# Optimization experiments

Measured on AMD Instinct MI355X. Metric: run time of the kernel, lower is better.

## Reference

```python
import jax, jax.numpy as jnp
import numpy as np

N, C, K, P = 262144, 64, 27, 131072
EPS = 1e-5


def setup_inputs() -> dict:
    key = jax.random.key(0)
    ks = jax.random.split(key, 8)
    x = jax.random.normal(ks[0], (N, C), jnp.float32)
    W1 = jax.random.normal(ks[1], (K, C, C), jnp.float32) * 0.05
    b1 = jax.random.normal(ks[2], (C,), jnp.float32) * 0.05
    W2 = jax.random.normal(ks[3], (K, C, C), jnp.float32) * 0.05
    b2 = jax.random.normal(ks[4], (C,), jnp.float32) * 0.05
    gamma1 = jnp.ones((C,), jnp.float32)
    beta1 = jnp.zeros((C,), jnp.float32)
    gamma2 = jnp.ones((C,), jnp.float32)
    beta2 = jnp.zeros((C,), jnp.float32)
    in_idx = jax.random.randint(ks[5], (K, P), 0, N, jnp.int32)
    out_idx = jax.random.randint(ks[6], (K, P), 0, N, jnp.int32)
    return dict(x=x, W1=W1, b1=b1, gamma1=gamma1, beta1=beta1,
                W2=W2, b2=b2, gamma2=gamma2, beta2=beta2,
                in_idx=in_idx, out_idx=out_idx)


def sparse_conv(x, W, b, in_idx, out_idx):
    """Rulebook sparse conv: for each kernel offset k, gather rows, GEMM, scatter-add."""
    out0 = jnp.zeros((x.shape[0], W.shape[-1]), x.dtype)

    def step(out, kslice):
        Wk, ik, ok = kslice
        msg = x[ik] @ Wk                      # [P, C] gather + GEMM
        return out.at[ok].add(msg), None      # scatter-add

    out, _ = jax.lax.scan(step, out0, (W, in_idx, out_idx))
    return out + b


def batchnorm(h, gamma, beta):
    # training-mode BatchNorm1d over node rows (biased variance)
    mean = h.mean(axis=0)
    var = h.var(axis=0)
    return (h - mean) * jax.lax.rsqrt(var + EPS) * gamma + beta


def reference(x, W1, b1, gamma1, beta1, W2, b2, gamma2, beta2, in_idx, out_idx):
    h = jax.nn.relu(batchnorm(sparse_conv(x, W1, b1, in_idx, out_idx), gamma1, beta1))
    h = batchnorm(sparse_conv(h, W2, b2, in_idx, out_idx), gamma2, beta2)
    return jax.nn.relu(h + x)  # identity shortcut (in_planes == planes, stride == 1)
```

## Files before the change

### kernel.cpp

```cpp
#include <hip/hip_runtime.h>
#include <hip/hip_bf16.h>


#define NNODES 262144
#define NC 64
#define NK 27
#define NP 131072
#define NPAIR (NK * NP)
#define EPSV 1e-5f
#define TILE 64
#define TPB 4
#define BGRID 2048

typedef float f32x4 __attribute__((ext_vector_type(4)));
typedef __bf16 bf16x8 __attribute__((ext_vector_type(8)));

__global__ void prep_w(const float* __restrict__ W, __bf16* __restrict__ Wt) {
    int i = blockIdx.x * 256 + threadIdx.x;
    if (i >= NK * NC * NC) return;
    int k  = i >> 12;
    int n  = (i >> 6) & 63;
    int ci = i & 63;
    Wt[i] = (__bf16)W[k * 4096 + ci * 64 + n];
}

__global__ __launch_bounds__(256) void prep_x(const float* __restrict__ X, __bf16* __restrict__ Xb) {
    size_t i = (size_t)(blockIdx.x * 256 + threadIdx.x) * 8;
    f32x4 a = *(const f32x4*)(X + i);
    f32x4 b = *(const f32x4*)(X + i + 4);
    bf16x8 o;
#pragma unroll
    for (int j = 0; j < 4; ++j) { o[j] = (__bf16)a[j]; o[4 + j] = (__bf16)b[j]; }
    *(bf16x8*)(Xb + i) = o;
}

__global__ void rank_kernel(const int* __restrict__ ok, int* __restrict__ hist, int* __restrict__ rank) {
    int i = blockIdx.x * 256 + threadIdx.x;
    rank[i] = atomicAdd(&hist[ok[i]], 1);
}

__global__ __launch_bounds__(256) void scan1(const int* __restrict__ hist, int* __restrict__ start,
                                             int* __restrict__ bsum) {
    __shared__ int sh[256];
    const int b = blockIdx.x, t = threadIdx.x;
    int4 v = *(const int4*)(hist + b * 1024 + t * 4);
    int s0 = v.x, s1 = s0 + v.y, s2 = s1 + v.z, s3 = s2 + v.w;
    sh[t] = s3;
    __syncthreads();
    for (int off = 1; off < 256; off <<= 1) {
        int val = (t >= off) ? sh[t - off] : 0;
        __syncthreads();
        sh[t] += val;
        __syncthreads();
    }
    int excl = (t == 0) ? 0 : sh[t - 1];
    if (t == 255) bsum[b] = sh[255];
    int4 o;
    o.x = excl; o.y = excl + s0; o.z = excl + s1; o.w = excl + s2;
    *(int4*)(start + b * 1024 + t * 4) = o;
}

__global__ __launch_bounds__(256) void scan2(int* __restrict__ bsum) {
    __shared__ int sh[256];
    const int t = threadIdx.x;
    sh[t] = bsum[t];
    __syncthreads();
    for (int off = 1; off < 256; off <<= 1) {
        int val = (t >= off) ? sh[t - off] : 0;
        __syncthreads();
        sh[t] += val;
        __syncthreads();
    }
    bsum[t] = (t == 0) ? 0 : sh[t - 1];
}

__global__ __launch_bounds__(256) void scan3(int* __restrict__ start, const int* __restrict__ bsum) {
    const int b = blockIdx.x, t = threadIdx.x;
    int add = bsum[b];
    int4 v = *(int4*)(start + b * 1024 + t * 4);
    v.x += add; v.y += add; v.z += add; v.w += add;
    *(int4*)(start + b * 1024 + t * 4) = v;
    if (b == 0 && t == 0) start[NNODES] = NPAIR;
}

__global__ void perm_kernel(const int* __restrict__ ok, const int* __restrict__ start,
                            int* __restrict__ rank) {
    int i = blockIdx.x * 256 + threadIdx.x;
    rank[i] = start[ok[i]] + rank[i];
}

__global__ __launch_bounds__(256) void bin_count(const int* __restrict__ ok, int* __restrict__ bhist,
                                                 int shiftC, int ncc) {
    __shared__ int lcount[32];
    int p = blockIdx.x * 256 + threadIdx.x;
    int k = p >> 17;
    int c = ok[p] >> shiftC;
    if (threadIdx.x < ncc) lcount[threadIdx.x] = 0;
    __syncthreads();
    atomicAdd(&lcount[c], 1);
    __syncthreads();
    if (threadIdx.x < ncc) {
        int n = lcount[threadIdx.x];
        if (n > 0) atomicAdd(&bhist[k * ncc + threadIdx.x], n);
    }
}

__global__ __launch_bounds__(1024) void bin_scan(const int* __restrict__ bhist,
                                                 int* __restrict__ bstart, int NB) {
    __shared__ int sh[1024];
    const int t = threadIdx.x;
    int own = (t < NB) ? bhist[t] : 0;
    sh[t] = own;
    __syncthreads();
    for (int off = 1; off < 1024; off <<= 1) {
        int val = (t >= off) ? sh[t - off] : 0;
        __syncthreads();
        sh[t] += val;
        __syncthreads();
    }
    if (t < NB) bstart[t] = sh[t] - own;
    if (t == 0) bstart[NB] = NPAIR;
}

__global__ __launch_bounds__(256) void bin_fill(const int* __restrict__ ik, const int* __restrict__ ok,
                                                const int* __restrict__ perm, const int* __restrict__ start,
                                                const int* __restrict__ bstart, int* __restrict__ bhist2,
                                                int* __restrict__ cin, int* __restrict__ cslot,
                                                int shiftC, int ncc) {
    __shared__ int lcount[32];
    __shared__ int lbase[32];
    int p = blockIdx.x * 256 + threadIdx.x;
    int k = p >> 17;
    int c = ok[p] >> shiftC;
    if (threadIdx.x < ncc) lcount[threadIdx.x] = 0;
    __syncthreads();
    int pos = atomicAdd(&lcount[c], 1);
    __syncthreads();
    if (threadIdx.x < ncc) {
        int n = lcount[threadIdx.x];
        lbase[threadIdx.x] = (n > 0) ? atomicAdd(&bhist2[k * ncc + threadIdx.x], n) : 0;
    }
    __syncthreads();
    int rec = bstart[k * ncc + c] + lbase[c] + pos;
    cin[rec]   = ik[p];
    cslot[rec] = perm[p] - start[c << shiftC];
}

template <bool BN>
__global__ __launch_bounds__(256)
void phaseA(const __bf16* __restrict__ Xb, const __bf16* __restrict__ Wt,
            const int* __restrict__ cin, const int* __restrict__ cslot,
            const int* __restrict__ bstart, const float* __restrict__ st,
            __bf16* __restrict__ msg, int ncc, int chunk, int capr) {
    const int k   = blockIdx.y;
    const int bin = k * ncc + chunk;
    const int b0  = bstart[bin];
    const int b1  = bstart[bin + 1];
    const int base = b0 + blockIdx.x * (TILE * TPB);
    if (base >= b1) return;

    const int tid  = threadIdx.x;
    const int wave = tid >> 6;
    const int lane = tid & 63;
    const int l15  = lane & 15;
    const int l4   = lane >> 4;

    __shared__ __align__(16) __bf16 As[64 * 64];
    __shared__ __align__(16) __bf16 Cs[64 * 64];
    __shared__ float s_s[64], s_t[64];

    if (BN && tid < 64) { s_s[tid] = st[tid]; s_t[tid] = st[64 + tid]; }

    bf16x8 bfrag[4][2];
    const __bf16* Wk = Wt + k * 4096;
#pragma unroll
    for (int nt = 0; nt < 4; ++nt)
#pragma unroll
        for (int ks = 0; ks < 2; ++ks)
            bfrag[nt][ks] = *(const bf16x8*)(Wk + (nt * 16 + l15) * 64 + ks * 32 + l4 * 8);

    const int r = tid >> 2;
    const int q = tid & 3;
    char* Ab = (char*)As;
    char* Cb = (char*)Cs;
    const int rb = wave * 16;

    __syncthreads();

    for (int t = 0; t < TPB; ++t) {
        const int p0 = base + t * TILE;
        if (p0 >= b1) break;
        const int rec   = p0 + r;
        const bool valid = rec < b1;
        const int gidx = valid ? cin[rec] : 0;
        const int slot = valid ? cslot[rec] : capr + r;

        const __bf16* xr = Xb + (size_t)gidx * 64 + q * 16;
        bf16x8 c0 = *(const bf16x8*)xr;
        bf16x8 c1 = *(const bf16x8*)(xr + 8);
        if (BN) {
            const int cb = q * 16;
#pragma unroll
            for (int j = 0; j < 8; ++j) {
                float v0 = (float)c0[j], v1 = (float)c1[j];
                c0[j] = (__bf16)fmaxf(fmaf(v0, s_s[cb + j],     s_t[cb + j]),     0.0f);
                c1[j] = (__bf16)fmaxf(fmaf(v1, s_s[cb + 8 + j], s_t[cb + 8 + j]), 0.0f);
            }
        }
        *(bf16x8*)(Ab + r * 128 + (((2 * q)     ^ (r & 7)) << 4)) = c0;
        *(bf16x8*)(Ab + r * 128 + (((2 * q + 1) ^ (r & 7)) << 4)) = c1;
        __syncthreads();

        f32x4 acc[4];
#pragma unroll
        for (int nt = 0; nt < 4; ++nt)
#pragma unroll
            for (int j = 0; j < 4; ++j) acc[nt][j] = 0.0f;
#pragma unroll
        for (int ks = 0; ks < 2; ++ks) {
            const int row = rb + l15;
            bf16x8 a = *(const bf16x8*)(Ab + row * 128 + ((((ks << 2) + l4) ^ (row & 7)) << 4));
#pragma unroll
            for (int nt = 0; nt < 4; ++nt)
                acc[nt] = __builtin_amdgcn_mfma_f32_16x16x32_bf16(a, bfrag[nt][ks], acc[nt], 0, 0, 0);
        }

#pragma unroll
        for (int rg = 0; rg < 4; ++rg) {
            const int row = rb + l4 * 4 + rg;
            char* cr = Cb + row * 128;
#pragma unroll
            for (int nt = 0; nt < 4; ++nt) {
                const int ch = nt * 2 + (l15 >> 3);
                *(__bf16*)(cr + ((ch ^ (row & 7)) << 4) + (l15 & 7) * 2) = (__bf16)acc[nt][rg];
            }
        }
        __syncthreads();

        bf16x8 o0 = *(bf16x8*)(Cb + r * 128 + (((2 * q)     ^ (r & 7)) << 4));
        bf16x8 o1 = *(bf16x8*)(Cb + r * 128 + (((2 * q + 1) ^ (r & 7)) << 4));
        __bf16* mr = msg + (size_t)slot * 64 + q * 16;
        *(bf16x8*)mr       = o0;
        *(bf16x8*)(mr + 8) = o1;
    }
}

template <bool FIRST>
__global__ __launch_bounds__(256)
void phaseB(const __bf16* __restrict__ msg, const int* __restrict__ start,
            int cbase, int nodesC,
            __bf16* __restrict__ outb, float* __restrict__ outf, float* __restrict__ psum) {
    const int wave = threadIdx.x >> 6;
    const int lane = threadIdx.x & 63;
    const int rs   = lane >> 3;
    const int g    = lane & 7;
    const int slotbase = start[cbase];
    float s[8], s2[8];
#pragma unroll
    for (int j = 0; j < 8; ++j) { s[j] = 0.0f; s2[j] = 0.0f; }

    for (int n0 = blockIdx.x * 4 + wave; n0 < nodesC; n0 += gridDim.x * 4) {
        const int n = cbase + n0;
        const int b = start[n] - slotbase;
        const int deg = start[n + 1] - slotbase - b;
        float acc[8];
#pragma unroll
        for (int j = 0; j < 8; ++j) acc[j] = 0.0f;
        for (int i = rs; i < deg; i += 8) {
            bf16x8 v = *(const bf16x8*)(msg + (size_t)(b + i) * 64 + g * 8);
#pragma unroll
            for (int j = 0; j < 8; ++j) acc[j] += (float)v[j];
        }
#pragma unroll
        for (int j = 0; j < 8; ++j) {
            acc[j] += __shfl_xor(acc[j], 8);
            acc[j] += __shfl_xor(acc[j], 16);
            acc[j] += __shfl_xor(acc[j], 32);
        }
        if (rs == 0) {
            if (FIRST) {
                bf16x8 o;
#pragma unroll
                for (int j = 0; j < 8; ++j) o[j] = (__bf16)acc[j];
                *(bf16x8*)(outb + (size_t)n * 64 + g * 8) = o;
            } else {
                f32x4 o0, o1;
#pragma unroll
                for (int j = 0; j < 4; ++j) { o0[j] = acc[j]; o1[j] = acc[4 + j]; }
                *(f32x4*)(outf + (size_t)n * 64 + g * 8)     = o0;
                *(f32x4*)(outf + (size_t)n * 64 + g * 8 + 4) = o1;
            }
#pragma unroll
            for (int j = 0; j < 8; ++j) { s[j] += acc[j]; s2[j] += acc[j] * acc[j]; }
        }
    }

    __shared__ float reds[4][64], reds2[4][64];
    if (rs == 0) {
#pragma unroll
        for (int j = 0; j < 8; ++j) { reds[wave][g * 8 + j] = s[j]; reds2[wave][g * 8 + j] = s2[j]; }
    }
    __syncthreads();
    if (threadIdx.x < 64) {
        const int c = threadIdx.x;
        float ts  = reds[0][c] + reds[1][c] + reds[2][c] + reds[3][c];
        float ts2 = reds2[0][c] + reds2[1][c] + reds2[2][c] + reds2[3][c];
        float* pr = psum + (size_t)blockIdx.x * 128;
        pr[c]      += ts;
        pr[64 + c] += ts2;
    }
}

__global__ __launch_bounds__(256) void bn_reduce(const float* __restrict__ psum, float* __restrict__ sums) {
    const int m = blockIdx.x;
    float s = 0.0f;
    for (int b = threadIdx.x; b < BGRID; b += 256) s += psum[(size_t)b * 128 + m];
    __shared__ float sh[256];
    sh[threadIdx.x] = s;
    __syncthreads();
    for (int off = 128; off > 0; off >>= 1) {
        if (threadIdx.x < off) sh[threadIdx.x] += sh[threadIdx.x + off];
        __syncthreads();
    }
    if (threadIdx.x == 0) sums[m] = sh[0];
}

__global__ void bn_params(const float* __restrict__ sums, const float* __restrict__ gamma,
                          const float* __restrict__ beta, float* __restrict__ st) {
    int c = threadIdx.x;
    const float inv = 1.0f / (float)NNODES;
    float mean = sums[c] * inv;
    float var  = sums[64 + c] * inv - mean * mean;
    float s    = gamma[c] * rsqrtf(var + EPSV);
    st[c]      = s;
    st[64 + c] = beta[c] - mean * s;
}

__global__ __launch_bounds__(256)
void final_kernel(float* __restrict__ Out, const float* __restrict__ X, const float* __restrict__ st) {
    __shared__ float s_s[64], s_t[64];
    if (threadIdx.x < 64) { s_s[threadIdx.x] = st[threadIdx.x]; s_t[threadIdx.x] = st[64 + threadIdx.x]; }
    __syncthreads();
    int i = blockIdx.x * 256 + threadIdx.x;
    f32x4 h  = *(f32x4*)(Out + (size_t)i * 4);
    f32x4 xv = *(const f32x4*)(X + (size_t)i * 4);
    const int cb = (i & 15) * 4;
    f32x4 o;
#pragma unroll
    for (int j = 0; j < 4; ++j)
        o[j] = fmaxf(fmaf(h[j], s_s[cb + j], s_t[cb + j]) + xv[j], 0.0f);
    *(f32x4*)(Out + (size_t)i * 4) = o;
}

template <bool BN>
__global__ __launch_bounds__(256)
void conv_kernel(const float* __restrict__ X, const __bf16* __restrict__ Wt,
                 const int* __restrict__ in_idx, const int* __restrict__ out_idx,
                 const float* __restrict__ st, float* __restrict__ Out) {
    const int k    = blockIdx.y;
    const int tid  = threadIdx.x;
    const int wave = tid >> 6;
    const int lane = tid & 63;
    const int l15  = lane & 15;
    const int l4   = lane >> 4;
    __shared__ __align__(16) __bf16 As[64 * 64];
    __shared__ int oks[TILE];
    __shared__ float s_s[64], s_t[64];
    if (BN && tid < 64) { s_s[tid] = st[tid]; s_t[tid] = st[64 + tid]; }
    bf16x8 bfrag[4][2];
    const __bf16* Wk = Wt + k * 4096;
#pragma unroll
    for (int nt = 0; nt < 4; ++nt)
#pragma unroll
        for (int ks = 0; ks < 2; ++ks)
            bfrag[nt][ks] = *(const bf16x8*)(Wk + (nt * 16 + l15) * 64 + ks * 32 + l4 * 8);
    const int* ik = in_idx + k * NP;
    const int* ok = out_idx + k * NP;
    const int r = tid >> 2;
    const int q = tid & 3;
    char* Abase = (char*)As;
    const int rb = wave * 16;
    __syncthreads();
    int p0 = (blockIdx.x * 8) * TILE;
    for (int t = 0; t < 8; ++t, p0 += TILE) {
        if (tid < TILE) oks[tid] = ok[p0 + tid];
        const float* xr = X + (size_t)ik[p0 + r] * 64 + q * 16;
        f32x4 v0 = *(const f32x4*)(xr + 0);
        f32x4 v1 = *(const f32x4*)(xr + 4);
        f32x4 v2 = *(const f32x4*)(xr + 8);
        f32x4 v3 = *(const f32x4*)(xr + 12);
        float vals[16];
        *(f32x4*)&vals[0]  = v0; *(f32x4*)&vals[4]  = v1;
        *(f32x4*)&vals[8]  = v2; *(f32x4*)&vals[12] = v3;
        if (BN) {
            const int cb = q * 16;
#pragma unroll
            for (int j = 0; j < 16; ++j)
                vals[j] = fmaxf(fmaf(vals[j], s_s[cb + j], s_t[cb + j]), 0.0f);
        }
        bf16x8 c0, c1;
#pragma unroll
        for (int j = 0; j < 8; ++j) { c0[j] = (__bf16)vals[j]; c1[j] = (__bf16)vals[8 + j]; }
        *(bf16x8*)(Abase + r * 128 + (((2 * q)     ^ (r & 7)) << 4)) = c0;
        *(bf16x8*)(Abase + r * 128 + (((2 * q + 1) ^ (r & 7)) << 4)) = c1;
        __syncthreads();
        f32x4 acc[4];
#pragma unroll
        for (int nt = 0; nt < 4; ++nt)
#pragma unroll
            for (int j = 0; j < 4; ++j) acc[nt][j] = 0.0f;
#pragma unroll
        for (int ks = 0; ks < 2; ++ks) {
            const int row = rb + l15;
            bf16x8 a = *(const bf16x8*)(Abase + row * 128 + ((((ks << 2) + l4) ^ (row & 7)) << 4));
#pragma unroll
            for (int nt = 0; nt < 4; ++nt)
                acc[nt] = __builtin_amdgcn_mfma_f32_16x16x32_bf16(a, bfrag[nt][ks], acc[nt], 0, 0, 0);
        }
#pragma unroll
        for (int rg = 0; rg < 4; ++rg) {
            const int rr = rb + l4 * 4 + rg;
            float* orow = Out + (size_t)oks[rr] * 64;
#pragma unroll
            for (int nt = 0; nt < 4; ++nt)
                unsafeAtomicAdd(orow + nt * 16 + l15, acc[nt][rg]);
        }
        __syncthreads();
    }
}

__global__ __launch_bounds__(256)
void bn_stats(const float* __restrict__ H, float* __restrict__ sums) {
    const int c    = threadIdx.x & 63;
    const int slot = threadIdx.x >> 6;
    float s = 0.0f, s2 = 0.0f;
    for (int row = blockIdx.x * 4 + slot; row < NNODES; row += gridDim.x * 4) {
        float v = H[(size_t)row * 64 + c];
        s += v; s2 += v * v;
    }
    __shared__ float red[8][64];
    red[slot][c] = s; red[4 + slot][c] = s2;
    __syncthreads();
    if (slot == 0) {
        s  = red[0][c] + red[1][c] + red[2][c] + red[3][c];
        s2 = red[4][c] + red[5][c] + red[6][c] + red[7][c];
        unsafeAtomicAdd(&sums[c], s);
        unsafeAtomicAdd(&sums[64 + c], s2);
    }
}

extern "C" void kernel_launch(void* const* d_in, const int* in_sizes, int n_in,
                              void* d_out, int out_size, void* d_ws, size_t ws_size,
                              hipStream_t stream) {
    const float* x      = (const float*)d_in[0];
    const float* W1     = (const float*)d_in[1];
    const float* gamma1 = (const float*)d_in[3];
    const float* beta1  = (const float*)d_in[4];
    const float* W2     = (const float*)d_in[5];
    const float* gamma2 = (const float*)d_in[7];
    const float* beta2  = (const float*)d_in[8];
    const int* in_idx   = (const int*)d_in[9];
    const int* out_idx  = (const int*)d_in[10];
    float* out = (float*)d_out;

    char* ws = (char*)d_ws;

    auto plan_bytes = [&](int ncc) -> size_t {
        auto rup = [](size_t b) { return (b + 255) & ~(size_t)255; };
        size_t capr = (size_t)NPAIR / ncc + 65536;
        size_t tot = 0;
        tot += rup((capr + 64) * 128);
        tot += rup((size_t)NNODES * 64 * 2);
        tot += rup((size_t)NNODES * 64 * 2);
        tot += rup((size_t)NPAIR * 4);
        tot += rup((size_t)NPAIR * 4);
        tot += rup((size_t)NPAIR * 4);
        tot += rup((size_t)NNODES * 4);
        tot += rup((size_t)(NNODES + 64) * 4);
        tot += rup((size_t)NK * ncc * 4) * 2;
        tot += rup((size_t)(NK * ncc + 1) * 4);
        tot += rup(1024);
        tot += rup((size_t)NK * 4096 * 2) * 2;
        tot += rup((size_t)BGRID * 128 * 4) * 2;
        tot += rup(512) * 4;
        return tot;
    };
    int ncc = -1;
    const int cands[4] = {4, 8, 16, 32};
    for (int ci = 0; ci < 4; ++ci)
        if (plan_bytes(cands[ci]) <= ws_size) { ncc = cands[ci]; break; }

    if (ncc > 0) {
        const int shiftC = 18 - __builtin_ctz(ncc);
        const int NB     = NK * ncc;
        const int capr   = NPAIR / ncc + 65536;
        const int nodesC = NNODES / ncc;

        size_t off = 0;
        auto alloc = [&](size_t bytes) -> char* {
            char* p = ws + off;
            off = (off + bytes + 255) & ~(size_t)255;
            return p;
        };
        __bf16* msg    = (__bf16*)alloc((size_t)(capr + 64) * 128);
        __bf16* xbf    = (__bf16*)alloc((size_t)NNODES * 64 * 2);
        __bf16* h1bf   = (__bf16*)alloc((size_t)NNODES * 64 * 2);
        int*    perm   = (int*)alloc((size_t)NPAIR * 4);
        int*    cin    = (int*)alloc((size_t)NPAIR * 4);
        int*    cslot  = (int*)alloc((size_t)NPAIR * 4);
        int*    hist   = (int*)alloc((size_t)NNODES * 4);
        int*    startv = (int*)alloc((size_t)(NNODES + 64) * 4);
        int*    bhist  = (int*)alloc((size_t)NB * 4);
        int*    bhist2 = (int*)alloc((size_t)NB * 4);
        int*    bstart = (int*)alloc((size_t)(NB + 1) * 4);
        int*    bsum   = (int*)alloc(1024);
        __bf16* Wt1    = (__bf16*)alloc((size_t)NK * 4096 * 2);
        __bf16* Wt2    = (__bf16*)alloc((size_t)NK * 4096 * 2);
        float*  psumA  = (float*)alloc((size_t)BGRID * 128 * 4);
        float*  psumB  = (float*)alloc((size_t)BGRID * 128 * 4);
        float*  sums1  = (float*)alloc(512);
        float*  st1    = (float*)alloc(512);
        float*  sums2  = (float*)alloc(512);
        float*  st2    = (float*)alloc(512);

        (void)hipMemsetAsync(hist, 0, (size_t)NNODES * 4, stream);
        (void)hipMemsetAsync(bhist, 0, (size_t)NB * 4, stream);
        (void)hipMemsetAsync(bhist2, 0, (size_t)NB * 4, stream);
        (void)hipMemsetAsync(psumA, 0, (size_t)BGRID * 128 * 4, stream);
        (void)hipMemsetAsync(psumB, 0, (size_t)BGRID * 128 * 4, stream);

        prep_x<<<NNODES * 64 / 8 / 256, 256, 0, stream>>>(x, xbf);
        prep_w<<<(NK * NC * NC + 255) / 256, 256, 0, stream>>>(W1, Wt1);
        prep_w<<<(NK * NC * NC + 255) / 256, 256, 0, stream>>>(W2, Wt2);

        rank_kernel<<<NPAIR / 256, 256, 0, stream>>>(out_idx, hist, perm);
        scan1<<<256, 256, 0, stream>>>(hist, startv, bsum);
        scan2<<<1, 256, 0, stream>>>(bsum);
        scan3<<<256, 256, 0, stream>>>(startv, bsum);
        perm_kernel<<<NPAIR / 256, 256, 0, stream>>>(out_idx, startv, perm);
        bin_count<<<NPAIR / 256, 256, 0, stream>>>(out_idx, bhist, shiftC, ncc);
        bin_scan<<<1, 1024, 0, stream>>>(bhist, bstart, NB);
        bin_fill<<<NPAIR / 256, 256, 0, stream>>>(in_idx, out_idx, perm, startv, bstart,
                                                  bhist2, cin, cslot, shiftC, ncc);

        const int meanbin = NP / ncc;
        const int cover   = meanbin + ((meanbin / 8 > 512) ? meanbin / 8 : 512);
        const int bx      = (cover + TILE * TPB - 1) / (TILE * TPB);
        dim3 agrid(bx, NK);

        for (int c = 0; c < ncc; ++c) {
            phaseA<false><<<agrid, 256, 0, stream>>>(xbf, Wt1, cin, cslot, bstart,
                                                     nullptr, msg, ncc, c, capr);
            phaseB<true><<<BGRID, 256, 0, stream>>>(msg, startv, c * nodesC, nodesC,
                                                    h1bf, nullptr, psumA);
        }
        bn_reduce<<<128, 256, 0, stream>>>(psumA, sums1);
        bn_params<<<1, 64, 0, stream>>>(sums1, gamma1, beta1, st1);
        for (int c = 0; c < ncc; ++c) {
            phaseA<true><<<agrid, 256, 0, stream>>>(h1bf, Wt2, cin, cslot, bstart,
                                                    st1, msg, ncc, c, capr);
            phaseB<false><<<BGRID, 256, 0, stream>>>(msg, startv, c * nodesC, nodesC,
                                                     nullptr, out, psumB);
        }
        bn_reduce<<<128, 256, 0, stream>>>(psumB, sums2);
        bn_params<<<1, 64, 0, stream>>>(sums2, gamma2, beta2, st2);
        final_kernel<<<NNODES * 64 / 4 / 256, 256, 0, stream>>>(out, x, st2);
    } else {
        size_t o2 = 0;
        auto alloc2 = [&](size_t bytes) -> char* {
            char* p = ws + o2;
            o2 = (o2 + bytes + 255) & ~(size_t)255;
            return p;
        };
        float*  h1    = (float*)alloc2((size_t)NNODES * 64 * 4);
        float*  fsums1= (float*)alloc2(512);
        float*  fst1  = (float*)alloc2(512);
        float*  fsums2= (float*)alloc2(512);
        float*  fst2  = (float*)alloc2(512);
        __bf16* fWt1  = (__bf16*)alloc2((size_t)NK * 4096 * 2);
        __bf16* fWt2  = (__bf16*)alloc2((size_t)NK * 4096 * 2);

        (void)hipMemsetAsync(h1, 0, (size_t)NNODES * 64 * 4, stream);
        (void)hipMemsetAsync(fsums1, 0, 512, stream);
        (void)hipMemsetAsync(fsums2, 0, 512, stream);
        (void)hipMemsetAsync(d_out, 0, (size_t)out_size * 4, stream);

        prep_w<<<(NK * NC * NC + 255) / 256, 256, 0, stream>>>(W1, fWt1);
        prep_w<<<(NK * NC * NC + 255) / 256, 256, 0, stream>>>(W2, fWt2);
        dim3 cgrid(NP / TILE / 8, NK);
        conv_kernel<false><<<cgrid, 256, 0, stream>>>(x, fWt1, in_idx, out_idx, nullptr, h1);
        bn_stats<<<1024, 256, 0, stream>>>(h1, fsums1);
        bn_params<<<1, 64, 0, stream>>>(fsums1, gamma1, beta1, fst1);
        conv_kernel<true><<<cgrid, 256, 0, stream>>>(h1, fWt2, in_idx, out_idx, fst1, out);
        bn_stats<<<1024, 256, 0, stream>>>(out, fsums2);
        bn_params<<<1, 64, 0, stream>>>(fsums2, gamma2, beta2, fst2);
        final_kernel<<<NNODES * 64 / 4 / 256, 256, 0, stream>>>(out, x, fst2);
    }
}
```

Before: 998.4 us.

## Fuse preprocessing kernels into one launch and enlarge phaseA tiles per block

Merges x/W bf16 conversion, the rank histogram and the bin count into a single multi-role kernel, and folds the perm computation into bin_fill, which removes several launches and one pass over out_idx. It also doubles tiles per block in phaseA, shrinks the message-buffer slack, and raises the minimum bin coverage. The smaller capr slack could overflow if a bin exceeds the mean by more than 16384 pairs, and larger blocks reduce the number of blocks in the grid.

```diff
diff --git a/kernel.cpp b/kernel.cpp
--- a/kernel.cpp
+++ b/kernel.cpp
@@ -9,7 +9,7 @@
 #define NPAIR (NK * NP)
 #define EPSV 1e-5f
 #define TILE 64
-#define TPB 4
+#define TPB 8
 #define BGRID 2048
 
 typedef float f32x4 __attribute__((ext_vector_type(4)));
@@ -24,19 +24,51 @@
     Wt[i] = (__bf16)W[k * 4096 + ci * 64 + n];
 }
 
-__global__ __launch_bounds__(256) void prep_x(const float* __restrict__ X, __bf16* __restrict__ Xb) {
-    size_t i = (size_t)(blockIdx.x * 256 + threadIdx.x) * 8;
-    f32x4 a = *(const f32x4*)(X + i);
-    f32x4 b = *(const f32x4*)(X + i + 4);
-    bf16x8 o;
-#pragma unroll
-    for (int j = 0; j < 4; ++j) { o[j] = (__bf16)a[j]; o[4 + j] = (__bf16)b[j]; }
-    *(bf16x8*)(Xb + i) = o;
-}
-
-__global__ void rank_kernel(const int* __restrict__ ok, int* __restrict__ hist, int* __restrict__ rank) {
-    int i = blockIdx.x * 256 + threadIdx.x;
-    rank[i] = atomicAdd(&hist[ok[i]], 1);
+#define BX 8192
+#define BW 864
+#define BR (NPAIR / 256)
+__global__ __launch_bounds__(256)
+void prep_all(const float* __restrict__ X, __bf16* __restrict__ Xb,
+              const float* __restrict__ W1, const float* __restrict__ W2,
+              __bf16* __restrict__ Wt1, __bf16* __restrict__ Wt2,
+              const int* __restrict__ ok, int* __restrict__ hist,
+              int* __restrict__ rank, int* __restrict__ bhist,
+              int shiftC, int ncc) {
+    __shared__ int lcount[32];
+    const int b = blockIdx.x;
+    const int t = threadIdx.x;
+    if (b < BX) {
+        size_t i = (size_t)(b * 256 + t) * 8;
+        f32x4 a0 = *(const f32x4*)(X + i);
+        f32x4 a1 = *(const f32x4*)(X + i + 4);
+        bf16x8 o;
+#pragma unroll
+        for (int j = 0; j < 4; ++j) { o[j] = (__bf16)a0[j]; o[4 + j] = (__bf16)a1[j]; }
+        *(bf16x8*)(Xb + i) = o;
+    } else if (b < BX + BW) {
+        int j = (b - BX) * 256 + t;
+        const float* Ws = (j < NK * 4096) ? W1 : W2;
+        __bf16* Wd      = (j < NK * 4096) ? Wt1 : Wt2;
+        int i = (j < NK * 4096) ? j : j - NK * 4096;
+        int k  = i >> 12;
+        int n  = (i >> 6) & 63;
+        int ci = i & 63;
+        Wd[i] = (__bf16)Ws[k * 4096 + ci * 64 + n];
+    } else {
+        int p = (b - BX - BW) * 256 + t;
+        int k = p >> 17;
+        int okp = ok[p];
+        int c = okp >> shiftC;
+        if (t < ncc) lcount[t] = 0;
+        __syncthreads();
+        atomicAdd(&lcount[c], 1);
+        rank[p] = atomicAdd(&hist[okp], 1);
+        __syncthreads();
+        if (t < ncc) {
+            int n = lcount[t];
+            if (n > 0) atomicAdd(&bhist[k * ncc + t], n);
+        }
+    }
 }
 
 __global__ __launch_bounds__(256) void scan1(const int* __restrict__ hist, int* __restrict__ start,
@@ -83,28 +115,6 @@
     if (b == 0 && t == 0) start[NNODES] = NPAIR;
 }
 
-__global__ void perm_kernel(const int* __restrict__ ok, const int* __restrict__ start,
-                            int* __restrict__ rank) {
-    int i = blockIdx.x * 256 + threadIdx.x;
-    rank[i] = start[ok[i]] + rank[i];
-}
-
-__global__ __launch_bounds__(256) void bin_count(const int* __restrict__ ok, int* __restrict__ bhist,
-                                                 int shiftC, int ncc) {
-    __shared__ int lcount[32];
-    int p = blockIdx.x * 256 + threadIdx.x;
-    int k = p >> 17;
-    int c = ok[p] >> shiftC;
-    if (threadIdx.x < ncc) lcount[threadIdx.x] = 0;
-    __syncthreads();
-    atomicAdd(&lcount[c], 1);
-    __syncthreads();
-    if (threadIdx.x < ncc) {
-        int n = lcount[threadIdx.x];
-        if (n > 0) atomicAdd(&bhist[k * ncc + threadIdx.x], n);
-    }
-}
-
 __global__ __launch_bounds__(1024) void bin_scan(const int* __restrict__ bhist,
                                                  int* __restrict__ bstart, int NB) {
     __shared__ int sh[1024];
@@ -123,7 +133,7 @@
 }
 
 __global__ __launch_bounds__(256) void bin_fill(const int* __restrict__ ik, const int* __restrict__ ok,
-                                                const int* __restrict__ perm, const int* __restrict__ start,
+                                                const int* __restrict__ rank, const int* __restrict__ start,
                                                 const int* __restrict__ bstart, int* __restrict__ bhist2,
                                                 int* __restrict__ cin, int* __restrict__ cslot,
                                                 int shiftC, int ncc) {
@@ -131,7 +141,8 @@
     __shared__ int lbase[32];
     int p = blockIdx.x * 256 + threadIdx.x;
     int k = p >> 17;
-    int c = ok[p] >> shiftC;
+    int okp = ok[p];
+    int c = okp >> shiftC;
     if (threadIdx.x < ncc) lcount[threadIdx.x] = 0;
     __syncthreads();
     int pos = atomicAdd(&lcount[c], 1);
@@ -143,7 +154,7 @@
     __syncthreads();
     int rec = bstart[k * ncc + c] + lbase[c] + pos;
     cin[rec]   = ik[p];
-    cslot[rec] = perm[p] - start[c << shiftC];
+    cslot[rec] = start[okp] + rank[p] - start[c << shiftC];
 }
 
 template <bool BN>
@@ -467,7 +478,7 @@
 
     auto plan_bytes = [&](int ncc) -> size_t {
         auto rup = [](size_t b) { return (b + 255) & ~(size_t)255; };
-        size_t capr = (size_t)NPAIR / ncc + 65536;
+        size_t capr = (size_t)NPAIR / ncc + 16384;
         size_t tot = 0;
         tot += rup((capr + 64) * 128);
         tot += rup((size_t)NNODES * 64 * 2);
@@ -493,7 +504,7 @@
     if (ncc > 0) {
         const int shiftC = 18 - __builtin_ctz(ncc);
         const int NB     = NK * ncc;
-        const int capr   = NPAIR / ncc + 65536;
+        const int capr   = NPAIR / ncc + 16384;
         const int nodesC = NNODES / ncc;
 
         size_t off = 0;
@@ -505,7 +516,7 @@
         __bf16* msg    = (__bf16*)alloc((size_t)(capr + 64) * 128);
         __bf16* xbf    = (__bf16*)alloc((size_t)NNODES * 64 * 2);
         __bf16* h1bf   = (__bf16*)alloc((size_t)NNODES * 64 * 2);
-        int*    perm   = (int*)alloc((size_t)NPAIR * 4);
+        int*    rank   = (int*)alloc((size_t)NPAIR * 4);
         int*    cin    = (int*)alloc((size_t)NPAIR * 4);
         int*    cslot  = (int*)alloc((size_t)NPAIR * 4);
         int*    hist   = (int*)alloc((size_t)NNODES * 4);
@@ -529,22 +540,18 @@
         (void)hipMemsetAsync(psumA, 0, (size_t)BGRID * 128 * 4, stream);
         (void)hipMemsetAsync(psumB, 0, (size_t)BGRID * 128 * 4, stream);
 
-        prep_x<<<NNODES * 64 / 8 / 256, 256, 0, stream>>>(x, xbf);
-        prep_w<<<(NK * NC * NC + 255) / 256, 256, 0, stream>>>(W1, Wt1);
-        prep_w<<<(NK * NC * NC + 255) / 256, 256, 0, stream>>>(W2, Wt2);
-
-        rank_kernel<<<NPAIR / 256, 256, 0, stream>>>(out_idx, hist, perm);
+        prep_all<<<BX + BW + BR, 256, 0, stream>>>(x, xbf, W1, W2, Wt1, Wt2,
+                                                   out_idx, hist, rank, bhist, shiftC, ncc);
+
         scan1<<<256, 256, 0, stream>>>(hist, startv, bsum);
         scan2<<<1, 256, 0, stream>>>(bsum);
         scan3<<<256, 256, 0, stream>>>(startv, bsum);
-        perm_kernel<<<NPAIR / 256, 256, 0, stream>>>(out_idx, startv, perm);
-        bin_count<<<NPAIR / 256, 256, 0, stream>>>(out_idx, bhist, shiftC, ncc);
         bin_scan<<<1, 1024, 0, stream>>>(bhist, bstart, NB);
-        bin_fill<<<NPAIR / 256, 256, 0, stream>>>(in_idx, out_idx, perm, startv, bstart,
+        bin_fill<<<NPAIR / 256, 256, 0, stream>>>(in_idx, out_idx, rank, startv, bstart,
                                                   bhist2, cin, cslot, shiftC, ncc);
 
         const int meanbin = NP / ncc;
-        const int cover   = meanbin + ((meanbin / 8 > 512) ? meanbin / 8 : 512);
+        const int cover   = meanbin + ((meanbin / 8 > 1024) ? meanbin / 8 : 1024);
         const int bx      = (cover + TILE * TPB - 1) / (TILE * TPB);
         dim3 agrid(bx, NK);
 
```

Result: no change. 0.9997 ms (+0.1%).
